# Kernel tuning notes

Measured on AMD Instinct MI355X. Metric: run time of the kernel, lower is better.

The kernel has to match this reference:

```python
import jax, jax.numpy as jnp
import numpy as np
import math

B, L, D, N = 8, 2048, 1024, 16

def setup_inputs() -> dict:
    key = jax.random.key(0)
    ks = jax.random.split(key, 6)
    x = jax.random.normal(ks[0], (B, L, D), dtype=jnp.float32)
    # A_log init: log(arange(1..N)) broadcast to (D, N)
    A_log = jnp.broadcast_to(jnp.log(jnp.arange(1, N + 1, dtype=jnp.float32))[None, :], (D, N))
    D_param = jnp.ones((D,), dtype=jnp.float32)
    s = 1.0 / math.sqrt(D)
    W_B = jax.random.uniform(ks[1], (N, D), minval=-s, maxval=s, dtype=jnp.float32)
    W_C = jax.random.uniform(ks[2], (N, D), minval=-s, maxval=s, dtype=jnp.float32)
    W_delta = jax.random.uniform(ks[3], (D, D), minval=-s, maxval=s, dtype=jnp.float32)
    b_delta = jax.random.uniform(ks[4], (D,), minval=math.log(0.001), maxval=math.log(0.1), dtype=jnp.float32)
    return {"x": x, "A_log": A_log, "D_param": D_param, "W_B": W_B,
            "W_C": W_C, "W_delta": W_delta, "b_delta": b_delta}

def reference(x, A_log, D_param, W_B, W_C, W_delta, b_delta):
    # x: (B, L, D)
    A = -jnp.exp(A_log)                                   # (D, N)
    B_in = jnp.einsum('bld,nd->bln', x, W_B)              # (B, L, N)
    C_in = jnp.einsum('bld,nd->bln', x, W_C)              # (B, L, N)
    delta = jax.nn.softplus(jnp.einsum('bld,ed->ble', x, W_delta) + b_delta)  # (B, L, D)
    h0 = jnp.zeros((x.shape[0], x.shape[2], A.shape[1]), dtype=x.dtype)       # (B, D, N)

    def step(h, inp):
        x_t, B_t, C_t, d_t = inp                          # (B,D),(B,N),(B,N),(B,D)
        A_bar = jnp.exp(d_t[:, :, None] * A[None])        # (B, D, N)
        h = A_bar * h + (d_t * x_t)[:, :, None] * B_t[:, None, :]
        y_t = jnp.einsum('bdn,bn->bd', h, C_t) + D_param * x_t
        return h, y_t

    xs = (jnp.swapaxes(x, 0, 1), jnp.swapaxes(B_in, 0, 1),
          jnp.swapaxes(C_in, 0, 1), jnp.swapaxes(delta, 0, 1))  # time-major
    h_final, ys = jax.lax.scan(step, h0, xs)
    y = jnp.swapaxes(ys, 0, 1)                            # (B, L, D)
    return y, h_final
```

## Files before the change

kernel.cpp:

```cpp
#include <hip/hip_runtime.h>
#include <hip/hip_bf16.h>
#include <math.h>

#define BB 8
#define LL 2048
#define DD 1024
#define NN 16
#define NC 64
#define LC 32

typedef __attribute__((ext_vector_type(8))) short bf16x8;
typedef __attribute__((ext_vector_type(4))) float f32x4;
typedef unsigned short u16;

__device__ __forceinline__ u16 f2bf(float f) {
  unsigned int u = __float_as_uint(f);
  u = (u + 0x7fffu + ((u >> 16) & 1u)) >> 16;
  return (u16)u;
}
__device__ __forceinline__ float bf2f(u16 v) {
  return __uint_as_float(((unsigned int)v) << 16);
}

__device__ __forceinline__ void gload16(const void* g, void* l) {
  __builtin_amdgcn_global_load_lds(
      (const __attribute__((address_space(1))) void*)g,
      (__attribute__((address_space(3))) void*)l, 16, 0, 0);
}

template <int N>
__device__ __forceinline__ void waitcnt_vm() {
  asm volatile("s_waitcnt vmcnt(%0)" ::"n"(N) : "memory");
  __builtin_amdgcn_sched_barrier(0);
}

__device__ __forceinline__ void pow_tree(float u, float* ab) {
  ab[0] = u;          ab[1] = u * u;       ab[2] = ab[1] * u;    ab[3] = ab[1] * ab[1];
  ab[4] = ab[3] * u;  ab[5] = ab[3] * ab[1]; ab[6] = ab[3] * ab[2]; ab[7] = ab[3] * ab[3];
  ab[8] = ab[7] * u;  ab[9] = ab[7] * ab[1]; ab[10] = ab[7] * ab[2]; ab[11] = ab[7] * ab[3];
  ab[12] = ab[7] * ab[4]; ab[13] = ab[7] * ab[5]; ab[14] = ab[7] * ab[6]; ab[15] = ab[7] * ab[7];
}

#define XN  (BB * LL * DD)
#define WDN (DD * DD)
#define WBN (NN * DD)

__global__ __launch_bounds__(256) void cvt_all(
    const float* __restrict__ x, const float* __restrict__ Wd,
    const float* __restrict__ WB, const float* __restrict__ WC,
    u16* __restrict__ xbf, u16* __restrict__ wdbf, u16* __restrict__ wbc) {
  size_t i = ((size_t)blockIdx.x * 256 + threadIdx.x) * 8;
  const float* src; u16* dst; size_t o;
  if (i < XN)                  { src = x;  dst = xbf;        o = i; }
  else if (i < XN + WDN)       { src = Wd; dst = wdbf;       o = i - XN; }
  else if (i < XN + WDN + WBN) { src = WB; dst = wbc;        o = i - XN - WDN; }
  else                         { src = WC; dst = wbc + WBN;  o = i - XN - WDN - WBN; }
  float4 a = *reinterpret_cast<const float4*>(src + o);
  float4 b = *reinterpret_cast<const float4*>(src + o + 4);
  ushort4 lo, hi;
  lo.x = f2bf(a.x); lo.y = f2bf(a.y); lo.z = f2bf(a.z); lo.w = f2bf(a.w);
  hi.x = f2bf(b.x); hi.y = f2bf(b.y); hi.z = f2bf(b.z); hi.w = f2bf(b.w);
  *reinterpret_cast<ushort4*>(dst + o) = lo;
  *reinterpret_cast<ushort4*>(dst + o + 4) = hi;
}

#define PHASE(CBUF, CKH, MH, SBUF, SKH, SI, SKT, SGUARD, WAITSTMT)            \
  {                                                                           \
    WAITSTMT;                                                                 \
    __builtin_amdgcn_s_barrier();                                             \
    bf16x8 af[4], bfr[4];                                                     \
    _Pragma("unroll")                                                         \
    for (int mf = 0; mf < 4; ++mf) {                                          \
      const int r = wr + ((MH) * 4 + mf) * 16 + l15;                          \
      af[mf] = *reinterpret_cast<const bf16x8*>(                              \
          &As[CBUF][CKH][r * 32 + (q ^ rdsw) * 8]);                           \
    }                                                                         \
    _Pragma("unroll")                                                         \
    for (int nf = 0; nf < 4; ++nf) {                                          \
      const int r = wc + nf * 16 + l15;                                       \
      bfr[nf] = *reinterpret_cast<const bf16x8*>(                             \
          &Bs[CBUF][CKH][r * 32 + (q ^ rdsw) * 8]);                           \
    }                                                                         \
    if (SGUARD) STG((SBUF), (SKH), (SI), (SKT));                              \
    __builtin_amdgcn_s_barrier();                                             \
    __builtin_amdgcn_s_setprio(1);                                            \
    _Pragma("unroll")                                                         \
    for (int mf = 0; mf < 4; ++mf) {                                          \
      _Pragma("unroll")                                                       \
      for (int nf = 0; nf < 4; ++nf)                                          \
        acc[(MH) * 4 + mf][nf] = __builtin_amdgcn_mfma_f32_16x16x32_bf16(     \
            af[mf], bfr[nf], acc[(MH) * 4 + mf][nf], 0, 0, 0);                \
    }                                                                         \
    __builtin_amdgcn_s_setprio(0);                                            \
  }

__global__ __launch_bounds__(512, 1) void gemm_delta_8ph(
    const u16* __restrict__ xb, const u16* __restrict__ wb,
    const float* __restrict__ bd, u16* deltabf, float* deltaf, int dbf16) {
  __shared__ u16 As[2][2][256 * 32];
  __shared__ u16 Bs[2][2][256 * 32];
  const int tid = threadIdx.x;
  const int wave = tid >> 6, lane = tid & 63;
  const int m0 = blockIdx.x * 256, n0 = blockIdx.y * 256;
  const int wr = (wave >> 2) * 128, wc = (wave & 3) * 64;
  const int l15 = lane & 15, q = lane >> 4;
  const int rdsw = (l15 >> 1) & 3;
  const int srow = lane >> 2;
  const int skol = ((lane & 3) ^ ((lane >> 3) & 3)) * 8;

  f32x4 acc[8][4];
#pragma unroll
  for (int i = 0; i < 8; ++i)
#pragma unroll
    for (int j = 0; j < 4; ++j) acc[i][j] = (f32x4){0.f, 0.f, 0.f, 0.f};

  auto STG = [&](int sbuf, int skh, int si, int skt) {
    const int gr = si * 128 + wave * 16;
    gload16(&xb[(size_t)(m0 + gr + srow) * 1024 + skt * 64 + skh * 32 + skol],
            &As[sbuf][skh][gr * 32]);
    gload16(&wb[(size_t)(n0 + gr + srow) * 1024 + skt * 64 + skh * 32 + skol],
            &Bs[sbuf][skh][gr * 32]);
  };

  STG(0, 0, 0, 0); STG(0, 0, 1, 0);
  STG(0, 1, 0, 0); STG(0, 1, 1, 0);
  STG(1, 0, 0, 1); STG(1, 0, 1, 1);

#pragma unroll 1
  for (int j = 0; j < 8; ++j) {
    const bool st = (j < 7);
    const int ktb = 2 * j + 1, kna = 2 * j + 2, knb = 2 * j + 3;
    PHASE(0, 0, 0, 1, 1, 0, ktb, true, waitcnt_vm<8>())
    PHASE(0, 0, 1, 1, 1, 1, ktb, true, (void)0)
    PHASE(0, 1, 0, 0, 0, 0, kna, st,   waitcnt_vm<8>())
    PHASE(0, 1, 1, 0, 0, 1, kna, st,   (void)0)
    PHASE(1, 0, 0, 0, 1, 0, kna, st,   if (st) waitcnt_vm<8>(); else waitcnt_vm<4>())
    PHASE(1, 0, 1, 0, 1, 1, kna, st,   (void)0)
    PHASE(1, 1, 0, 1, 0, 0, knb, st,   if (st) waitcnt_vm<8>(); else waitcnt_vm<0>())
    PHASE(1, 1, 1, 1, 0, 1, knb, st,   (void)0)
  }

  const int crow = q * 4, ccol = l15;
#pragma unroll
  for (int mi = 0; mi < 8; ++mi) {
#pragma unroll
    for (int nf = 0; nf < 4; ++nf) {
      const int cn = n0 + wc + nf * 16 + ccol;
      const float bias = bd[cn];
#pragma unroll
      for (int r = 0; r < 4; ++r) {
        const size_t rm = (size_t)(m0 + wr + mi * 16 + crow + r);
        float v = acc[mi][nf][r] + bias;
        float sp = (v > 15.f) ? v : __logf(1.f + __expf(v));
        if (dbf16) deltabf[rm * 1024 + cn] = f2bf(sp);
        else       deltaf[rm * 1024 + cn] = sp;
      }
    }
  }
}

__global__ __launch_bounds__(256) void gemm_bc_mfma(
    const u16* __restrict__ xb, const u16* __restrict__ wbc,
    float* __restrict__ Bin, float* __restrict__ Cin) {
  __shared__ u16 As2[2][64 * 64];
  __shared__ u16 Ws[2][32 * 64];
  const int tid = threadIdx.x;
  const int wave = tid >> 6, lane = tid & 63;
  const int m0 = blockIdx.x * 64;
  const int srow = lane >> 3;
  const int skol = ((lane & 7) ^ srow) * 8;
  const int l15 = lane & 15, q = lane >> 4;

  f32x4 acc[2];
  acc[0] = (f32x4){0.f, 0.f, 0.f, 0.f};
  acc[1] = (f32x4){0.f, 0.f, 0.f, 0.f};

  auto STAGE = [&](int buf, int kb) {
#pragma unroll
    for (int s = 0; s < 2; ++s) {
      const int g = wave * 2 + s;
      gload16(&xb[(size_t)(m0 + g * 8 + srow) * 1024 + kb + skol], &As2[buf][g * 512]);
    }
    gload16(&wbc[(size_t)(wave * 8 + srow) * 1024 + kb + skol], &Ws[buf][wave * 512]);
  };

  auto COMPUTE = [&](int buf) {
#pragma unroll
    for (int kh = 0; kh < 2; ++kh) {
      bf16x8 af;
      {
        const int r = wave * 16 + l15;
        const int c = (kh * 4 + q) ^ (r & 7);
        af = *reinterpret_cast<const bf16x8*>(&As2[buf][r * 64 + c * 8]);
      }
#pragma unroll
      for (int nf = 0; nf < 2; ++nf) {
        const int r = nf * 16 + l15;
        const int c = (kh * 4 + q) ^ (r & 7);
        bf16x8 wf = *reinterpret_cast<const bf16x8*>(&Ws[buf][r * 64 + c * 8]);
        acc[nf] = __builtin_amdgcn_mfma_f32_16x16x32_bf16(af, wf, acc[nf], 0, 0, 0);
      }
    }
  };

  STAGE(0, 0);
  __syncthreads();
  for (int it = 0; it < 16; ++it) {
    const int cur = it & 1;
    if (it < 15) STAGE(cur ^ 1, (it + 1) * 64);
    COMPUTE(cur);
    __syncthreads();
  }

  const int crow = q * 4, ccol = l15;
#pragma unroll
  for (int r = 0; r < 4; ++r) {
    const size_t rm = (size_t)(m0 + wave * 16 + crow + r);
    Bin[rm * 16 + ccol] = acc[0][r];
    Cin[rm * 16 + ccol] = acc[1][r];
  }
}

template <int DBF>
__global__ __launch_bounds__(256) void scan_p1(
    const void* __restrict__ deltap, const u16* __restrict__ xbf,
    const float* __restrict__ Bin,
    float* __restrict__ sumd, u16* __restrict__ hloc) {
  const int d = blockIdx.x * 256 + threadIdx.x;
  const int c = blockIdx.y, b = blockIdx.z;
  const int t0 = c * LC;
  __shared__ float Bsh[LC][NN];
  for (int e = threadIdx.x; e < LC * NN; e += 256)
    Bsh[e / NN][e % NN] = Bin[(size_t)(b * LL + t0) * NN + e];
  __syncthreads();
  float h[NN] = {};
  float sd = 0.f;
  const size_t base = (size_t)(b * LL + t0) * DD + d;
  const u16* dpb = (const u16*)deltap + base;
  const float* dpf = (const float*)deltap + base;
  const u16* xp = xbf + base;
  float dt = DBF ? bf2f(dpb[0]) : dpf[0];
  float xt = bf2f(xp[0]);
  for (int t = 0; t < LC; ++t) {
    const int tn = (t + 1 < LC) ? t + 1 : t;
    float dtn = DBF ? bf2f(dpb[(size_t)tn * DD]) : dpf[(size_t)tn * DD];
    float xtn = bf2f(xp[(size_t)tn * DD]);
    sd += dt;
    float zb = dt * xt;
    float ab[NN];
    pow_tree(__expf(-dt), ab);
#pragma unroll
    for (int n = 0; n < NN; ++n)
      h[n] = fmaf(ab[n], h[n], zb * Bsh[t][n]);
    dt = dtn; xt = xtn;
  }
  sumd[((size_t)b * NC + c) * DD + d] = sd;
#pragma unroll
  for (int n = 0; n < NN; ++n)
    hloc[(((size_t)(b * NC + c)) * NN + n) * DD + d] = f2bf(h[n]);
}

__global__ __launch_bounds__(256) void scan_p2(
    const float* __restrict__ sumd, u16* __restrict__ h01,
    float* __restrict__ hfin) {
  const int g = blockIdx.x * 256 + threadIdx.x;
  const int d = g % DD;
  const int n = (g / DD) % NN;
  const int b = g / (DD * NN);
  const float A = -(float)(n + 1);
  float h = 0.f;
  for (int c = 0; c < NC; ++c) {
    const size_t base = (((size_t)(b * NC + c)) * NN + n) * DD + d;
    float hl = bf2f(h01[base]);
    h01[base] = f2bf(h);
    float a = __expf(A * sumd[((size_t)b * NC + c) * DD + d]);
    h = fmaf(a, h, hl);
  }
  hfin[((size_t)b * DD + d) * NN + n] = h;
}

template <int DBF>
__global__ __launch_bounds__(256) void scan_p3(
    const void* deltap, const u16* __restrict__ xbf,
    const float* __restrict__ Bin, const float* __restrict__ Cin,
    const float* __restrict__ Dp, const u16* __restrict__ h0, float* y) {
  const int d = blockIdx.x * 256 + threadIdx.x;
  const int c = blockIdx.y, b = blockIdx.z;
  const int t0 = c * LC;
  __shared__ float Bsh[LC][NN], Csh[LC][NN];
  for (int e = threadIdx.x; e < LC * NN; e += 256) {
    Bsh[e / NN][e % NN] = Bin[(size_t)(b * LL + t0) * NN + e];
    Csh[e / NN][e % NN] = Cin[(size_t)(b * LL + t0) * NN + e];
  }
  __syncthreads();
  float h[NN];
#pragma unroll
  for (int n = 0; n < NN; ++n)
    h[n] = bf2f(h0[(((size_t)(b * NC + c)) * NN + n) * DD + d]);
  const float Dpar = Dp[d];
  const size_t base = (size_t)(b * LL + t0) * DD + d;
  const u16* dpb = (const u16*)deltap + base;
  const float* dpf = (const float*)deltap + base;
  const u16* xp = xbf + base;
  float* yp = y + base;
  float dt = DBF ? bf2f(dpb[0]) : dpf[0];
  float xt = bf2f(xp[0]);
  for (int t = 0; t < LC; ++t) {
    const int tn = (t + 1 < LC) ? t + 1 : t;
    float dtn = DBF ? bf2f(dpb[(size_t)tn * DD]) : dpf[(size_t)tn * DD];
    float xtn = bf2f(xp[(size_t)tn * DD]);
    float zb = dt * xt;
    float acc = Dpar * xt;
    float ab[NN];
    pow_tree(__expf(-dt), ab);
#pragma unroll
    for (int n = 0; n < NN; ++n) {
      h[n] = fmaf(ab[n], h[n], zb * Bsh[t][n]);
      acc = fmaf(h[n], Csh[t][n], acc);
    }
    yp[(size_t)t * DD] = acc;
    dt = dtn; xt = xtn;
  }
}

extern "C" void kernel_launch(void* const* d_in, const int* in_sizes, int n_in,
                              void* d_out, int out_size, void* d_ws, size_t ws_size,
                              hipStream_t stream) {
  const float* x     = (const float*)d_in[0];
  const float* A_log = (const float*)d_in[1];
  const float* Dp    = (const float*)d_in[2];
  const float* WB    = (const float*)d_in[3];
  const float* WC    = (const float*)d_in[4];
  const float* Wd    = (const float*)d_in[5];
  const float* bd    = (const float*)d_in[6];
  (void)A_log;

  float* y    = (float*)d_out;
  float* hfin = y + (size_t)BB * LL * DD;

  float* w    = (float*)d_ws;
  float* Bin  = w;
  float* Cin  = Bin + (size_t)BB * LL * NN;
  float* sumd = Cin + (size_t)BB * LL * NN;
  u16* hloc   = (u16*)(sumd + (size_t)BB * NC * DD);
  u16* xbf    = hloc + (size_t)BB * NC * NN * DD;
  u16* wdbf   = xbf + (size_t)XN;
  u16* wbcbf  = wdbf + (size_t)WDN;
  u16* deltabf = wbcbf + 2 * WBN;

  const size_t need_bf = (size_t)((char*)(deltabf + (size_t)XN) - (char*)d_ws);
  const int dbf16 = (ws_size >= need_bf) ? 1 : 0;
  float* deltaf = y;

  cvt_all<<<dim3((XN + WDN + 2 * WBN) / 2048), 256, 0, stream>>>(
      x, Wd, WB, WC, xbf, wdbf, wbcbf);
  gemm_delta_8ph<<<dim3(BB * LL / 256, DD / 256), 512, 0, stream>>>(
      xbf, wdbf, bd, deltabf, deltaf, dbf16);
  gemm_bc_mfma<<<dim3(BB * LL / 64), 256, 0, stream>>>(xbf, wbcbf, Bin, Cin);
  const void* dp = dbf16 ? (const void*)deltabf : (const void*)deltaf;
  if (dbf16) {
    scan_p1<1><<<dim3(DD / 256, NC, BB), 256, 0, stream>>>(dp, xbf, Bin, sumd, hloc);
  } else {
    scan_p1<0><<<dim3(DD / 256, NC, BB), 256, 0, stream>>>(dp, xbf, Bin, sumd, hloc);
  }
  scan_p2<<<dim3(BB * NN * DD / 256), 256, 0, stream>>>(sumd, hloc, hfin);
  if (dbf16) {
    scan_p3<1><<<dim3(DD / 256, NC, BB), 256, 0, stream>>>(dp, xbf, Bin, Cin, Dp, hloc, y);
  } else {
    scan_p3<0><<<dim3(DD / 256, NC, BB), 256, 0, stream>>>(dp, xbf, Bin, Cin, Dp, hloc, y);
  }
}
```

Baseline: 158.1 us.

## Fuse x bf16 conversion into the B/C projection GEMM kernel

The fp32-to-bf16 conversion of x moves out of the standalone conversion kernel and into a new B/C GEMM. That GEMM reads fp32 x, converts it in registers, writes the bf16 copy for later kernels and also stages it into LDS for the MFMA projection. This removes one full pass that re-read xbf for the B/C GEMM. The new GEMM uses smaller K tiles with register double-buffering. A sched_barrier after vmcnt waits is also removed, which may change instruction scheduling in the delta GEMM.

```diff
diff --git a/kernel.cpp b/kernel.cpp
--- a/kernel.cpp
+++ b/kernel.cpp
@@ -31,7 +31,6 @@
 template <int N>
 __device__ __forceinline__ void waitcnt_vm() {
   asm volatile("s_waitcnt vmcnt(%0)" ::"n"(N) : "memory");
-  __builtin_amdgcn_sched_barrier(0);
 }
 
 __device__ __forceinline__ void pow_tree(float u, float* ab) {
@@ -45,16 +44,14 @@
 #define WDN (DD * DD)
 #define WBN (NN * DD)
 
-__global__ __launch_bounds__(256) void cvt_all(
-    const float* __restrict__ x, const float* __restrict__ Wd,
-    const float* __restrict__ WB, const float* __restrict__ WC,
-    u16* __restrict__ xbf, u16* __restrict__ wdbf, u16* __restrict__ wbc) {
+__global__ __launch_bounds__(256) void cvt_w(
+    const float* __restrict__ Wd, const float* __restrict__ WB,
+    const float* __restrict__ WC, u16* __restrict__ wdbf, u16* __restrict__ wbc) {
   size_t i = ((size_t)blockIdx.x * 256 + threadIdx.x) * 8;
   const float* src; u16* dst; size_t o;
-  if (i < XN)                  { src = x;  dst = xbf;        o = i; }
-  else if (i < XN + WDN)       { src = Wd; dst = wdbf;       o = i - XN; }
-  else if (i < XN + WDN + WBN) { src = WB; dst = wbc;        o = i - XN - WDN; }
-  else                         { src = WC; dst = wbc + WBN;  o = i - XN - WDN - WBN; }
+  if (i < WDN)            { src = Wd; dst = wdbf;      o = i; }
+  else if (i < WDN + WBN) { src = WB; dst = wbc;       o = i - WDN; }
+  else                    { src = WC; dst = wbc + WBN; o = i - WDN - WBN; }
   float4 a = *reinterpret_cast<const float4*>(src + o);
   float4 b = *reinterpret_cast<const float4*>(src + o + 4);
   ushort4 lo, hi;
@@ -62,6 +59,87 @@
   hi.x = f2bf(b.x); hi.y = f2bf(b.y); hi.z = f2bf(b.z); hi.w = f2bf(b.w);
   *reinterpret_cast<ushort4*>(dst + o) = lo;
   *reinterpret_cast<ushort4*>(dst + o + 4) = hi;
+}
+
+__global__ __launch_bounds__(256) void gemm_bcx(
+    const float* __restrict__ x, const u16* __restrict__ wbc,
+    u16* __restrict__ xbf, float* __restrict__ Bin, float* __restrict__ Cin) {
+  __shared__ u16 Xs[2][64 * 32];
+  __shared__ u16 Ws[2][32 * 32];
+  const int tid = threadIdx.x;
+  const int wave = tid >> 6, lane = tid & 63;
+  const int m0 = blockIdx.x * 64;
+  const int l15 = lane & 15, q = lane >> 4;
+  const int rdsw = (l15 >> 1) & 3;
+  const int xrow = tid >> 2;
+  const int xkc = (tid & 3) * 8;
+  const int xphys = (((tid & 3) ^ ((xrow >> 1) & 3)) & 3) * 8;
+  const int srow = lane >> 2;
+  const int skol = ((lane & 3) ^ ((lane >> 3) & 3)) * 8;
+
+  f32x4 acc0 = (f32x4){0.f, 0.f, 0.f, 0.f};
+  f32x4 acc1 = (f32x4){0.f, 0.f, 0.f, 0.f};
+
+  float4 rA0, rA1, rB0, rB1;
+  auto LOADA = [&](int kb) {
+    const float* p = &x[(size_t)(m0 + xrow) * 1024 + kb + xkc];
+    rA0 = *reinterpret_cast<const float4*>(p);
+    rA1 = *reinterpret_cast<const float4*>(p + 4);
+  };
+  auto LOADB = [&](int kb) {
+    const float* p = &x[(size_t)(m0 + xrow) * 1024 + kb + xkc];
+    rB0 = *reinterpret_cast<const float4*>(p);
+    rB1 = *reinterpret_cast<const float4*>(p + 4);
+  };
+  auto PUT = [&](const float4& r0, const float4& r1, int buf, int kb) {
+    union { ushort us[8]; uint4 v; } pk;
+    pk.us[0] = f2bf(r0.x); pk.us[1] = f2bf(r0.y);
+    pk.us[2] = f2bf(r0.z); pk.us[3] = f2bf(r0.w);
+    pk.us[4] = f2bf(r1.x); pk.us[5] = f2bf(r1.y);
+    pk.us[6] = f2bf(r1.z); pk.us[7] = f2bf(r1.w);
+    *reinterpret_cast<uint4*>(&Xs[buf][xrow * 32 + xphys]) = pk.v;
+    *reinterpret_cast<uint4*>(&xbf[(size_t)(m0 + xrow) * 1024 + kb + xkc]) = pk.v;
+  };
+  auto STW = [&](int buf, int kb) {
+    if (wave < 2)
+      gload16(&wbc[(size_t)(wave * 16 + srow) * 1024 + kb + skol],
+              &Ws[buf][wave * 512]);
+  };
+  auto COMP = [&](int buf) {
+    const int r = wave * 16 + l15;
+    bf16x8 af = *reinterpret_cast<const bf16x8*>(&Xs[buf][r * 32 + (q ^ rdsw) * 8]);
+    bf16x8 w0 = *reinterpret_cast<const bf16x8*>(&Ws[buf][l15 * 32 + (q ^ rdsw) * 8]);
+    bf16x8 w1 = *reinterpret_cast<const bf16x8*>(&Ws[buf][(16 + l15) * 32 + (q ^ rdsw) * 8]);
+    acc0 = __builtin_amdgcn_mfma_f32_16x16x32_bf16(af, w0, acc0, 0, 0, 0);
+    acc1 = __builtin_amdgcn_mfma_f32_16x16x32_bf16(af, w1, acc1, 0, 0, 0);
+  };
+
+  LOADA(0);
+  STW(0, 0);
+  for (int it = 0; it < 32; it += 2) {
+    if (it + 1 < 32) LOADB((it + 1) * 32);
+    PUT(rA0, rA1, 0, it * 32);
+    if (it + 1 < 32) STW(1, (it + 1) * 32);
+    __syncthreads();
+    COMP(0);
+    __syncthreads();
+    if (it + 1 < 32) {
+      if (it + 2 < 32) LOADA((it + 2) * 32);
+      PUT(rB0, rB1, 1, (it + 1) * 32);
+      if (it + 2 < 32) STW(0, (it + 2) * 32);
+      __syncthreads();
+      COMP(1);
+      __syncthreads();
+    }
+  }
+
+  const int crow = q * 4;
+#pragma unroll
+  for (int r = 0; r < 4; ++r) {
+    const size_t rm = (size_t)(m0 + wave * 16 + crow + r);
+    Bin[rm * 16 + l15] = acc0[r];
+    Cin[rm * 16 + l15] = acc1[r];
+  }
 }
 
 #define PHASE(CBUF, CKH, MH, SBUF, SKH, SI, SKT, SGUARD, WAITSTMT)            \
@@ -159,68 +237,6 @@
   }
 }
 
-__global__ __launch_bounds__(256) void gemm_bc_mfma(
-    const u16* __restrict__ xb, const u16* __restrict__ wbc,
-    float* __restrict__ Bin, float* __restrict__ Cin) {
-  __shared__ u16 As2[2][64 * 64];
-  __shared__ u16 Ws[2][32 * 64];
-  const int tid = threadIdx.x;
-  const int wave = tid >> 6, lane = tid & 63;
-  const int m0 = blockIdx.x * 64;
-  const int srow = lane >> 3;
-  const int skol = ((lane & 7) ^ srow) * 8;
-  const int l15 = lane & 15, q = lane >> 4;
-
-  f32x4 acc[2];
-  acc[0] = (f32x4){0.f, 0.f, 0.f, 0.f};
-  acc[1] = (f32x4){0.f, 0.f, 0.f, 0.f};
-
-  auto STAGE = [&](int buf, int kb) {
-#pragma unroll
-    for (int s = 0; s < 2; ++s) {
-      const int g = wave * 2 + s;
-      gload16(&xb[(size_t)(m0 + g * 8 + srow) * 1024 + kb + skol], &As2[buf][g * 512]);
-    }
-    gload16(&wbc[(size_t)(wave * 8 + srow) * 1024 + kb + skol], &Ws[buf][wave * 512]);
-  };
-
-  auto COMPUTE = [&](int buf) {
-#pragma unroll
-    for (int kh = 0; kh < 2; ++kh) {
-      bf16x8 af;
-      {
-        const int r = wave * 16 + l15;
-        const int c = (kh * 4 + q) ^ (r & 7);
-        af = *reinterpret_cast<const bf16x8*>(&As2[buf][r * 64 + c * 8]);
-      }
-#pragma unroll
-      for (int nf = 0; nf < 2; ++nf) {
-        const int r = nf * 16 + l15;
-        const int c = (kh * 4 + q) ^ (r & 7);
-        bf16x8 wf = *reinterpret_cast<const bf16x8*>(&Ws[buf][r * 64 + c * 8]);
-        acc[nf] = __builtin_amdgcn_mfma_f32_16x16x32_bf16(af, wf, acc[nf], 0, 0, 0);
-      }
-    }
-  };
-
-  STAGE(0, 0);
-  __syncthreads();
-  for (int it = 0; it < 16; ++it) {
-    const int cur = it & 1;
-    if (it < 15) STAGE(cur ^ 1, (it + 1) * 64);
-    COMPUTE(cur);
-    __syncthreads();
-  }
-
-  const int crow = q * 4, ccol = l15;
-#pragma unroll
-  for (int r = 0; r < 4; ++r) {
-    const size_t rm = (size_t)(m0 + wave * 16 + crow + r);
-    Bin[rm * 16 + ccol] = acc[0][r];
-    Cin[rm * 16 + ccol] = acc[1][r];
-  }
-}
-
 template <int DBF>
 __global__ __launch_bounds__(256) void scan_p1(
     const void* __restrict__ deltap, const u16* __restrict__ xbf,
@@ -352,11 +368,10 @@
   const int dbf16 = (ws_size >= need_bf) ? 1 : 0;
   float* deltaf = y;
 
-  cvt_all<<<dim3((XN + WDN + 2 * WBN) / 2048), 256, 0, stream>>>(
-      x, Wd, WB, WC, xbf, wdbf, wbcbf);
+  cvt_w<<<dim3((WDN + 2 * WBN) / 2048), 256, 0, stream>>>(Wd, WB, WC, wdbf, wbcbf);
+  gemm_bcx<<<dim3(BB * LL / 64), 256, 0, stream>>>(x, wbcbf, xbf, Bin, Cin);
   gemm_delta_8ph<<<dim3(BB * LL / 256, DD / 256), 512, 0, stream>>>(
       xbf, wdbf, bd, deltabf, deltaf, dbf16);
-  gemm_bc_mfma<<<dim3(BB * LL / 64), 256, 0, stream>>>(xbf, wbcbf, Bin, Cin);
   const void* dp = dbf16 ? (const void*)deltabf : (const void*)deltaf;
   if (dbf16) {
     scan_p1<1><<<dim3(DD / 256, NC, BB), 256, 0, stream>>>(dp, xbf, Bin, sumd, hloc);
```

New measurement: 158.5 us. No clear change (+0.2%).
